# Kernel tuning notes

Measured on AMD Instinct MI355X. Metric: run time of the kernel, lower is better.

## Reference

```python
import jax, jax.numpy as jnp
import numpy as np

EPS = 0.01
MAX_ITER = 10
H = W = 48
N = H * W
B = 16


def radial_cost_matrix():
    # pairwise Euclidean distance between pixel coordinates of an HxW grid,
    # normalized to [0, 1]; shape (1, N, N)
    ys, xs = np.meshgrid(np.arange(H), np.arange(W), indexing='ij')
    coords = np.stack([ys.ravel(), xs.ravel()], axis=1).astype(np.float32)  # (N, 2)
    d = np.sqrt(((coords[:, None, :] - coords[None, :, :]) ** 2).sum(-1))
    d = d / d.max()
    return d[None].astype(np.float32)


def setup_inputs() -> dict:
    key = jax.random.key(0)
    k1, k2 = jax.random.split(key)
    pred_logits = jax.random.normal(k1, (B, H, W), dtype=jnp.float32)
    t = jax.random.uniform(k2, (B, H, W), dtype=jnp.float32)
    target_probs = t / t.sum(axis=(1, 2), keepdims=True)  # valid probability maps
    C = jnp.asarray(radial_cost_matrix())  # (1, N, N) buffer, not trainable
    return {"pred_logits": pred_logits, "target_probs": target_probs, "C": C}


def _M(C, u, v):
    # M_ij = (-c_ij + u_i + v_j) / eps ; shapes: C (1,N,N), u,v (B,N) -> (B,N,N)
    return (-C + u[..., None] + v[..., None, :]) / EPS


def reference(pred_logits, target_probs, C):
    b = pred_logits.shape[0]
    pred_logp = jax.nn.log_softmax(pred_logits.reshape(b, -1), axis=1)  # (B, N)
    target_logp = jnp.log(target_probs.reshape(b, -1) + 1e-8)           # (B, N)

    u = jnp.zeros_like(pred_logp)
    v = jnp.zeros_like(target_logp)
    for _ in range(MAX_ITER):  # fixed small iteration count (no early exit)
        u = EPS * (pred_logp - jax.nn.logsumexp(_M(C, u, v), axis=-1)) + u
        v = EPS * (target_logp - jax.nn.logsumexp(_M(C, u, v), axis=-2)) + v

    pi = jnp.exp(_M(C, u, v))                      # (B, N, N) transport plan
    cost = jnp.sum(pi * C, axis=(-2, -1))           # (B,)
    return cost.mean()                              # reduction='mean'
```

## Files before the change

kernel.cpp:

```cpp
#include <hip/hip_runtime.h>


namespace {

constexpr int N    = 2304;
constexpr int B    = 16;
constexpr int NB   = N * B;
constexpr int R    = 16;
constexpr int WIN  = 33;
constexpr int WPAD = 36;
constexpr int RPB  = 3;
constexpr int AR   = RPB + 2 * R;
constexpr int AST  = 84;
constexpr int NOUT = RPB * 48;
constexpr int NTH  = 17 * 12;

__device__ __forceinline__ float wave_sum(float v) {
#pragma unroll
    for (int off = 32; off >= 1; off >>= 1) v += __shfl_xor(v, off);
    return v;
}

template <bool WC>
__device__ __forceinline__ void stage_wt(float* wtl, float* wcl,
                                         const float* __restrict__ C) {
    for (int i = threadIdx.x; i < WIN * WPAD; i += 256) {
        const int dy = i / WPAD, dx = i - dy * WPAD;
        float wv = 0.f, wc = 0.f;
        if (dx < WIN) {
            const float c = C[1176 * N + (8 + dy) * 48 + (8 + dx)];
            wv = __expf(c * -100.f);
            wc = wv * c;
        }
        wtl[i] = wv;
        if (WC) wcl[i] = wc;
    }
}

template <bool ONES>
__device__ __forceinline__ void stage_apron(float* vl, const float* win,
                                            int b, int y0) {
    for (int i = threadIdx.x; i < AR * 20; i += 256) {
        const int rr = i / 20, c4 = i - rr * 20;
        const int y = y0 - R + rr, x0 = c4 * 4 - R;
        float4 v = make_float4(0.f, 0.f, 0.f, 0.f);
        if ((unsigned)y < 48u && (unsigned)x0 < 48u)
            v = ONES ? make_float4(1.f, 1.f, 1.f, 1.f)
                     : *(const float4*)(win + b * N + y * 48 + x0);
        *(float4*)&vl[rr * AST + c4 * 4] = v;
    }
}

template <int MODE>
__global__ __launch_bounds__(256) void sk_pass(const float* __restrict__ logits,
                                               const float* __restrict__ target,
                                               const float* __restrict__ C,
                                               float* __restrict__ smstat,
                                               float* __restrict__ A,
                                               float* __restrict__ Bh,
                                               float* __restrict__ out) {
    __shared__ float vl[AR * AST];
    __shared__ float wtl[WIN * WPAD];
    __shared__ float part[NTH * 12];
    __shared__ float sred[8];

    const int bid = blockIdx.x;
    const int b   = bid & 15;
    const int y0  = (bid >> 4) * RPB;
    const int tid = threadIdx.x, w = tid >> 6, lane = tid & 63;

    stage_wt<false>(wtl, nullptr, C);
    stage_apron<MODE == 0>(vl, (MODE == 1) ? A : Bh, b, y0);

    float sm_m = 0.f, sm_inv = 0.f;
    if (MODE == 0) {
        float xs[9];
        float m = -3.0e38f;
#pragma unroll
        for (int s9 = 0; s9 < 9; ++s9) {
            xs[s9] = logits[b * N + s9 * 256 + tid];
            m = fmaxf(m, xs[s9]);
        }
#pragma unroll
        for (int off = 32; off >= 1; off >>= 1) m = fmaxf(m, __shfl_xor(m, off));
        if (lane == 0) sred[w] = m;
        __syncthreads();
        m = fmaxf(fmaxf(sred[0], sred[1]), fmaxf(sred[2], sred[3]));
        float sum = 0.f;
#pragma unroll
        for (int s9 = 0; s9 < 9; ++s9) sum += __expf(xs[s9] - m);
#pragma unroll
        for (int off = 32; off >= 1; off >>= 1) sum += __shfl_xor(sum, off);
        __syncthreads();
        if (lane == 0) sred[4 + w] = sum;
        __syncthreads();
        sum = sred[4] + sred[5] + sred[6] + sred[7];
        sm_m = m;
        sm_inv = 1.f / sum;
        if (tid == 0 && (bid >> 4) == 0) {
            smstat[2 * b]     = sm_m;
            smstat[2 * b + 1] = sm_inv;
            if (b == 0) out[0] = 0.f;
        }
    } else if (MODE == 2) {
        sm_m   = smstat[2 * b];
        sm_inv = smstat[2 * b + 1];
    }
    __syncthreads();

    if (tid < NTH) {
        const int dy2 = tid / 12, s = tid - dy2 * 12;
        const int r = s >> 2, xw = (s & 3) * 12;
        float acc[12];
#pragma unroll
        for (int k = 0; k < 12; ++k) acc[k] = 0.f;
#pragma unroll
        for (int h = 0; h < 2; ++h) {
            const int dy = 2 * dy2 + h;
            if (dy < WIN) {
                float vr[44], wr[36];
                const float* vp = &vl[(r + dy) * AST + xw];
#pragma unroll
                for (int c = 0; c < 11; ++c)
                    *(float4*)&vr[4 * c] = *(const float4*)&vp[4 * c];
                const float* wp = &wtl[dy * WPAD];
#pragma unroll
                for (int c = 0; c < 9; ++c)
                    *(float4*)&wr[4 * c] = *(const float4*)&wp[4 * c];
#pragma unroll
                for (int dx = 0; dx < WIN; ++dx)
#pragma unroll
                    for (int k = 0; k < 12; ++k)
                        acc[k] = fmaf(wr[dx], vr[k + dx], acc[k]);
            }
        }
#pragma unroll
        for (int c = 0; c < 3; ++c)
            *(float4*)&part[tid * 12 + 4 * c] = *(float4*)&acc[4 * c];
    }
    __syncthreads();

    if (tid < NOUT) {
        float ssum = 0.f;
#pragma unroll
        for (int d = 0; d < 17; ++d) ssum += part[d * 144 + tid];
        const int o = b * N + (y0 + tid / 48) * 48 + (tid % 48);
        float sv;
        if (MODE == 1) sv = target[o] + 1e-8f;
        else           sv = __expf(logits[o] - sm_m) * sm_inv;
        float* dst = (MODE == 1) ? Bh : A;
        dst[o] = sv / ssum;
    }
}

__global__ __launch_bounds__(256) void sk_cost(const float* __restrict__ C,
                                               const float* __restrict__ target,
                                               const float* __restrict__ A,
                                               float* __restrict__ out) {
    __shared__ float vl[AR * AST];
    __shared__ float wtl[WIN * WPAD], wcl[WIN * WPAD];
    __shared__ float p1[NTH * 12], p2[NTH * 12];
    __shared__ float sred[4];

    const int bid = blockIdx.x;
    const int b   = bid & 15;
    const int y0  = (bid >> 4) * RPB;
    const int tid = threadIdx.x, w = tid >> 6, lane = tid & 63;

    stage_wt<true>(wtl, wcl, C);
    stage_apron<false>(vl, A, b, y0);
    __syncthreads();

    if (tid < NTH) {
        const int dy2 = tid / 12, s = tid - dy2 * 12;
        const int r = s >> 2, xw = (s & 3) * 12;
        float a1[12], a2[12];
#pragma unroll
        for (int k = 0; k < 12; ++k) { a1[k] = 0.f; a2[k] = 0.f; }
#pragma unroll
        for (int h = 0; h < 2; ++h) {
            const int dy = 2 * dy2 + h;
            if (dy < WIN) {
                float vr[44], wr[36], cr[36];
                const float* vp = &vl[(r + dy) * AST + xw];
#pragma unroll
                for (int c = 0; c < 11; ++c)
                    *(float4*)&vr[4 * c] = *(const float4*)&vp[4 * c];
#pragma unroll
                for (int c = 0; c < 9; ++c) {
                    *(float4*)&wr[4 * c] = *(const float4*)&wtl[dy * WPAD + 4 * c];
                    *(float4*)&cr[4 * c] = *(const float4*)&wcl[dy * WPAD + 4 * c];
                }
#pragma unroll
                for (int dx = 0; dx < WIN; ++dx)
#pragma unroll
                    for (int k = 0; k < 12; ++k) {
                        a1[k] = fmaf(wr[dx], vr[k + dx], a1[k]);
                        a2[k] = fmaf(cr[dx], vr[k + dx], a2[k]);
                    }
            }
        }
#pragma unroll
        for (int c = 0; c < 3; ++c) {
            *(float4*)&p1[tid * 12 + 4 * c] = *(float4*)&a1[4 * c];
            *(float4*)&p2[tid * 12 + 4 * c] = *(float4*)&a2[4 * c];
        }
    }
    __syncthreads();

    float val = 0.f;
    if (tid < NOUT) {
        float s1 = 0.f, s2 = 0.f;
#pragma unroll
        for (int d = 0; d < 17; ++d) {
            s1 += p1[d * 144 + tid];
            s2 += p2[d * 144 + tid];
        }
        const int o = b * N + (y0 + tid / 48) * 48 + (tid % 48);
        val = (target[o] + 1e-8f) / s1 * s2;
    }
    val = wave_sum(val);
    if (lane == 0) sred[w] = val;
    __syncthreads();
    if (tid == 0)
        atomicAdd(out, (sred[0] + sred[1] + sred[2] + sred[3]) * (1.f / 16.f));
}

}

extern "C" void kernel_launch(void* const* d_in, const int* in_sizes, int n_in,
                              void* d_out, int out_size, void* d_ws, size_t ws_size,
                              hipStream_t stream) {
    const float* logits = (const float*)d_in[0];
    const float* target = (const float*)d_in[1];
    const float* C      = (const float*)d_in[2];
    float* out = (float*)d_out;
    float* ws  = (float*)d_ws;

    float* smstat = ws;
    float* A      = ws + 32;
    float* Bh     = A + NB;

    sk_pass<0><<<256, 256, 0, stream>>>(logits, target, C, smstat, A, Bh, out);

    for (int t = 1; t <= 9; ++t) {
        sk_pass<1><<<256, 256, 0, stream>>>(logits, target, C, smstat, A, Bh, out);
        sk_pass<2><<<256, 256, 0, stream>>>(logits, target, C, smstat, A, Bh, out);
    }

    sk_cost<<<256, 256, 0, stream>>>(C, target, A, out);
}
```

Measured before the change: 98.05 us.

## Fuse both Sinkhorn half-steps per iteration and shrink the kernel window radius

Each Sinkhorn iteration now runs in one kernel instead of two. The kernel recomputes the intermediate target-side scaling over a halo of rows in shared memory, then convolves it again to produce the next source-side scaling. This halves the number of launches and drops the global round trip for the intermediate buffer. The Gibbs kernel window also shrinks from radius 16 to radius 10, which cuts the FMA work per output. The cost is redundant halo computation of the intermediate rows in every block, plus extra truncation error from the smaller window.

```diff
diff --git a/kernel.cpp b/kernel.cpp
--- a/kernel.cpp
+++ b/kernel.cpp
@@ -6,14 +6,16 @@
 constexpr int N    = 2304;
 constexpr int B    = 16;
 constexpr int NB   = N * B;
-constexpr int R    = 16;
-constexpr int WIN  = 33;
-constexpr int WPAD = 36;
-constexpr int RPB  = 3;
-constexpr int AR   = RPB + 2 * R;
-constexpr int AST  = 84;
-constexpr int NOUT = RPB * 48;
-constexpr int NTH  = 17 * 12;
+constexpr int R    = 10;
+constexpr int WIN  = 21;
+constexpr int WPAD = 24;
+constexpr int APX  = 12;
+constexpr int AST  = 76;
+constexpr int NOUT = 144;
+constexpr int NTH  = WIN * 12;
+constexpr int AVR1 = 23;
+constexpr int AVR2 = 43;
+constexpr int BVR  = 23;
 
 __device__ __forceinline__ float wave_sum(float v) {
 #pragma unroll
@@ -28,7 +30,7 @@
         const int dy = i / WPAD, dx = i - dy * WPAD;
         float wv = 0.f, wc = 0.f;
         if (dx < WIN) {
-            const float c = C[1176 * N + (8 + dy) * 48 + (8 + dx)];
+            const float c = C[1176 * N + (14 + dy) * 48 + (14 + dx)];
             wv = __expf(c * -100.f);
             wc = wv * c;
         }
@@ -38,102 +40,87 @@
 }
 
 template <bool ONES>
-__device__ __forceinline__ void stage_apron(float* vl, const float* win,
-                                            int b, int y0) {
-    for (int i = threadIdx.x; i < AR * 20; i += 256) {
-        const int rr = i / 20, c4 = i - rr * 20;
-        const int y = y0 - R + rr, x0 = c4 * 4 - R;
+__device__ __forceinline__ void stage_ap(float* vl, const float* img,
+                                         int b, int ytop, int nrows) {
+    for (int i = threadIdx.x; i < nrows * 18; i += 256) {
+        const int rr = i / 18, c4 = i - rr * 18;
+        const int y = ytop + rr, x0 = c4 * 4 - APX;
         float4 v = make_float4(0.f, 0.f, 0.f, 0.f);
         if ((unsigned)y < 48u && (unsigned)x0 < 48u)
             v = ONES ? make_float4(1.f, 1.f, 1.f, 1.f)
-                     : *(const float4*)(win + b * N + y * 48 + x0);
+                     : *(const float4*)(img + b * N + y * 48 + x0);
         *(float4*)&vl[rr * AST + c4 * 4] = v;
     }
 }
 
-template <int MODE>
-__global__ __launch_bounds__(256) void sk_pass(const float* __restrict__ logits,
-                                               const float* __restrict__ target,
-                                               const float* __restrict__ C,
-                                               float* __restrict__ smstat,
-                                               float* __restrict__ A,
-                                               float* __restrict__ Bh,
-                                               float* __restrict__ out) {
-    __shared__ float vl[AR * AST];
+__device__ __forceinline__ void conv_row(const float* vp, const float* wp,
+                                         float* acc) {
+    float vr[36], wr[24];
+#pragma unroll
+    for (int c = 0; c < 9; ++c) *(float4*)&vr[4 * c] = *(const float4*)&vp[4 * c];
+#pragma unroll
+    for (int c = 0; c < 6; ++c) *(float4*)&wr[4 * c] = *(const float4*)&wp[4 * c];
+#pragma unroll
+    for (int dx = 0; dx < WIN; ++dx)
+#pragma unroll
+        for (int k = 0; k < 12; ++k)
+            acc[k] = fmaf(wr[dx], vr[k + 2 + dx], acc[k]);
+}
+
+__global__ __launch_bounds__(256) void sk_a1(const float* __restrict__ logits,
+                                             const float* __restrict__ C,
+                                             float* __restrict__ smstat,
+                                             float* __restrict__ A0,
+                                             float* __restrict__ out) {
+    __shared__ float vl[AVR1 * AST];
     __shared__ float wtl[WIN * WPAD];
     __shared__ float part[NTH * 12];
     __shared__ float sred[8];
 
     const int bid = blockIdx.x;
     const int b   = bid & 15;
-    const int y0  = (bid >> 4) * RPB;
+    const int y0  = (bid >> 4) * 3;
     const int tid = threadIdx.x, w = tid >> 6, lane = tid & 63;
 
     stage_wt<false>(wtl, nullptr, C);
-    stage_apron<MODE == 0>(vl, (MODE == 1) ? A : Bh, b, y0);
-
-    float sm_m = 0.f, sm_inv = 0.f;
-    if (MODE == 0) {
-        float xs[9];
-        float m = -3.0e38f;
-#pragma unroll
-        for (int s9 = 0; s9 < 9; ++s9) {
-            xs[s9] = logits[b * N + s9 * 256 + tid];
-            m = fmaxf(m, xs[s9]);
-        }
-#pragma unroll
-        for (int off = 32; off >= 1; off >>= 1) m = fmaxf(m, __shfl_xor(m, off));
-        if (lane == 0) sred[w] = m;
-        __syncthreads();
-        m = fmaxf(fmaxf(sred[0], sred[1]), fmaxf(sred[2], sred[3]));
-        float sum = 0.f;
-#pragma unroll
-        for (int s9 = 0; s9 < 9; ++s9) sum += __expf(xs[s9] - m);
-#pragma unroll
-        for (int off = 32; off >= 1; off >>= 1) sum += __shfl_xor(sum, off);
-        __syncthreads();
-        if (lane == 0) sred[4 + w] = sum;
-        __syncthreads();
-        sum = sred[4] + sred[5] + sred[6] + sred[7];
-        sm_m = m;
-        sm_inv = 1.f / sum;
-        if (tid == 0 && (bid >> 4) == 0) {
-            smstat[2 * b]     = sm_m;
-            smstat[2 * b + 1] = sm_inv;
-            if (b == 0) out[0] = 0.f;
-        }
-    } else if (MODE == 2) {
-        sm_m   = smstat[2 * b];
-        sm_inv = smstat[2 * b + 1];
+    stage_ap<true>(vl, nullptr, b, y0 - R, AVR1);
+
+    float xs[9];
+    float m = -3.0e38f;
+#pragma unroll
+    for (int s9 = 0; s9 < 9; ++s9) {
+        xs[s9] = logits[b * N + s9 * 256 + tid];
+        m = fmaxf(m, xs[s9]);
+    }
+#pragma unroll
+    for (int off = 32; off >= 1; off >>= 1) m = fmaxf(m, __shfl_xor(m, off));
+    if (lane == 0) sred[w] = m;
+    __syncthreads();
+    m = fmaxf(fmaxf(sred[0], sred[1]), fmaxf(sred[2], sred[3]));
+    float sum = 0.f;
+#pragma unroll
+    for (int s9 = 0; s9 < 9; ++s9) sum += __expf(xs[s9] - m);
+#pragma unroll
+    for (int off = 32; off >= 1; off >>= 1) sum += __shfl_xor(sum, off);
+    __syncthreads();
+    if (lane == 0) sred[4 + w] = sum;
+    __syncthreads();
+    sum = sred[4] + sred[5] + sred[6] + sred[7];
+    const float sm_m = m, sm_inv = 1.f / sum;
+    if (tid == 0 && (bid >> 4) == 0) {
+        smstat[2 * b]     = sm_m;
+        smstat[2 * b + 1] = sm_inv;
+        if (b == 0) out[0] = 0.f;
     }
     __syncthreads();
 
     if (tid < NTH) {
-        const int dy2 = tid / 12, s = tid - dy2 * 12;
-        const int r = s >> 2, xw = (s & 3) * 12;
+        const int dy = tid / 12, strip = tid - dy * 12;
+        const int r = strip >> 2, xw = (strip & 3) * 12;
         float acc[12];
 #pragma unroll
         for (int k = 0; k < 12; ++k) acc[k] = 0.f;
-#pragma unroll
-        for (int h = 0; h < 2; ++h) {
-            const int dy = 2 * dy2 + h;
-            if (dy < WIN) {
-                float vr[44], wr[36];
-                const float* vp = &vl[(r + dy) * AST + xw];
-#pragma unroll
-                for (int c = 0; c < 11; ++c)
-                    *(float4*)&vr[4 * c] = *(const float4*)&vp[4 * c];
-                const float* wp = &wtl[dy * WPAD];
-#pragma unroll
-                for (int c = 0; c < 9; ++c)
-                    *(float4*)&wr[4 * c] = *(const float4*)&wp[4 * c];
-#pragma unroll
-                for (int dx = 0; dx < WIN; ++dx)
-#pragma unroll
-                    for (int k = 0; k < 12; ++k)
-                        acc[k] = fmaf(wr[dx], vr[k + dx], acc[k]);
-            }
-        }
+        conv_row(&vl[(r + dy) * AST + xw], &wtl[dy * WPAD], acc);
 #pragma unroll
         for (int c = 0; c < 3; ++c)
             *(float4*)&part[tid * 12 + 4 * c] = *(float4*)&acc[4 * c];
@@ -143,63 +130,133 @@
     if (tid < NOUT) {
         float ssum = 0.f;
 #pragma unroll
-        for (int d = 0; d < 17; ++d) ssum += part[d * 144 + tid];
+        for (int d = 0; d < WIN; ++d) ssum += part[d * 144 + tid];
         const int o = b * N + (y0 + tid / 48) * 48 + (tid % 48);
-        float sv;
-        if (MODE == 1) sv = target[o] + 1e-8f;
-        else           sv = __expf(logits[o] - sm_m) * sm_inv;
-        float* dst = (MODE == 1) ? Bh : A;
-        dst[o] = sv / ssum;
-    }
-}
-
-__global__ __launch_bounds__(256) void sk_cost(const float* __restrict__ C,
-                                               const float* __restrict__ target,
-                                               const float* __restrict__ A,
+        A0[o] = __expf(logits[o] - sm_m) * sm_inv / ssum;
+    }
+}
+
+__global__ __launch_bounds__(256) void sk_fused(const float* __restrict__ logits,
+                                                const float* __restrict__ target,
+                                                const float* __restrict__ C,
+                                                const float* __restrict__ smstat,
+                                                const float* __restrict__ Ain,
+                                                float* __restrict__ Aout) {
+    __shared__ float vl[AVR2 * AST];
+    __shared__ float bv[BVR * AST];
+    __shared__ float wtl[WIN * WPAD];
+    __shared__ float part[NTH * 12];
+
+    const int bid = blockIdx.x;
+    const int b   = bid & 15;
+    const int y0  = (bid >> 4) * 3;
+    const int tid = threadIdx.x;
+
+    stage_wt<false>(wtl, nullptr, C);
+    stage_ap<false>(vl, Ain, b, y0 - 2 * R, AVR2);
+    for (int i = tid; i < BVR * AST; i += 256) bv[i] = 0.f;
+    const float sm_m = smstat[2 * b], sm_inv = smstat[2 * b + 1];
+    __syncthreads();
+
+    int dy = 0, r = 0, xw = 0;
+    const bool act = tid < NTH;
+    if (act) {
+        dy = tid / 12;
+        const int strip = tid - dy * 12;
+        r  = strip >> 2;
+        xw = (strip & 3) * 12;
+    }
+
+    for (int c = 0; c < 8; ++c) {
+        const int rb = 3 * c + r;
+        if (act && rb < BVR) {
+            float acc[12];
+#pragma unroll
+            for (int k = 0; k < 12; ++k) acc[k] = 0.f;
+            conv_row(&vl[(rb + dy) * AST + xw], &wtl[dy * WPAD], acc);
+#pragma unroll
+            for (int cc = 0; cc < 3; ++cc)
+                *(float4*)&part[tid * 12 + 4 * cc] = *(float4*)&acc[4 * cc];
+        }
+        __syncthreads();
+
+        const int nred = (c == 7) ? 96 : 144;
+        if (tid < nred) {
+            float ssum = 0.f;
+#pragma unroll
+            for (int d = 0; d < WIN; ++d) ssum += part[d * 144 + tid];
+            const int rb2 = 3 * c + tid / 48;
+            const int ybg = y0 - R + rb2;
+            const int x   = tid % 48;
+            if ((unsigned)ybg < 48u) {
+                const float q = target[b * N + ybg * 48 + x] + 1e-8f;
+                bv[rb2 * AST + APX + x] = q / ssum;
+            }
+        }
+        __syncthreads();
+    }
+
+    if (act) {
+        float acc[12];
+#pragma unroll
+        for (int k = 0; k < 12; ++k) acc[k] = 0.f;
+        conv_row(&bv[(r + dy) * AST + xw], &wtl[dy * WPAD], acc);
+#pragma unroll
+        for (int cc = 0; cc < 3; ++cc)
+            *(float4*)&part[tid * 12 + 4 * cc] = *(float4*)&acc[4 * cc];
+    }
+    __syncthreads();
+
+    if (tid < NOUT) {
+        float ssum = 0.f;
+#pragma unroll
+        for (int d = 0; d < WIN; ++d) ssum += part[d * 144 + tid];
+        const int o = b * N + (y0 + tid / 48) * 48 + (tid % 48);
+        Aout[o] = __expf(logits[o] - sm_m) * sm_inv / ssum;
+    }
+}
+
+__global__ __launch_bounds__(256) void sk_cost(const float* __restrict__ target,
+                                               const float* __restrict__ C,
+                                               const float* __restrict__ Ain,
                                                float* __restrict__ out) {
-    __shared__ float vl[AR * AST];
+    __shared__ float vl[AVR1 * AST];
     __shared__ float wtl[WIN * WPAD], wcl[WIN * WPAD];
     __shared__ float p1[NTH * 12], p2[NTH * 12];
     __shared__ float sred[4];
 
     const int bid = blockIdx.x;
     const int b   = bid & 15;
-    const int y0  = (bid >> 4) * RPB;
+    const int y0  = (bid >> 4) * 3;
     const int tid = threadIdx.x, w = tid >> 6, lane = tid & 63;
 
     stage_wt<true>(wtl, wcl, C);
-    stage_apron<false>(vl, A, b, y0);
+    stage_ap<false>(vl, Ain, b, y0 - R, AVR1);
     __syncthreads();
 
     if (tid < NTH) {
-        const int dy2 = tid / 12, s = tid - dy2 * 12;
-        const int r = s >> 2, xw = (s & 3) * 12;
+        const int dy = tid / 12, strip = tid - dy * 12;
+        const int r = strip >> 2, xw = (strip & 3) * 12;
         float a1[12], a2[12];
 #pragma unroll
         for (int k = 0; k < 12; ++k) { a1[k] = 0.f; a2[k] = 0.f; }
-#pragma unroll
-        for (int h = 0; h < 2; ++h) {
-            const int dy = 2 * dy2 + h;
-            if (dy < WIN) {
-                float vr[44], wr[36], cr[36];
-                const float* vp = &vl[(r + dy) * AST + xw];
-#pragma unroll
-                for (int c = 0; c < 11; ++c)
-                    *(float4*)&vr[4 * c] = *(const float4*)&vp[4 * c];
-#pragma unroll
-                for (int c = 0; c < 9; ++c) {
-                    *(float4*)&wr[4 * c] = *(const float4*)&wtl[dy * WPAD + 4 * c];
-                    *(float4*)&cr[4 * c] = *(const float4*)&wcl[dy * WPAD + 4 * c];
-                }
-#pragma unroll
-                for (int dx = 0; dx < WIN; ++dx)
-#pragma unroll
-                    for (int k = 0; k < 12; ++k) {
-                        a1[k] = fmaf(wr[dx], vr[k + dx], a1[k]);
-                        a2[k] = fmaf(cr[dx], vr[k + dx], a2[k]);
-                    }
+        float vr[36], wr[24], cr[24];
+        const float* vp = &vl[(r + dy) * AST + xw];
+#pragma unroll
+        for (int c = 0; c < 9; ++c)
+            *(float4*)&vr[4 * c] = *(const float4*)&vp[4 * c];
+#pragma unroll
+        for (int c = 0; c < 6; ++c) {
+            *(float4*)&wr[4 * c] = *(const float4*)&wtl[dy * WPAD + 4 * c];
+            *(float4*)&cr[4 * c] = *(const float4*)&wcl[dy * WPAD + 4 * c];
+        }
+#pragma unroll
+        for (int dx = 0; dx < WIN; ++dx)
+#pragma unroll
+            for (int k = 0; k < 12; ++k) {
+                a1[k] = fmaf(wr[dx], vr[k + 2 + dx], a1[k]);
+                a2[k] = fmaf(cr[dx], vr[k + 2 + dx], a2[k]);
             }
-        }
 #pragma unroll
         for (int c = 0; c < 3; ++c) {
             *(float4*)&p1[tid * 12 + 4 * c] = *(float4*)&a1[4 * c];
@@ -212,7 +269,7 @@
     if (tid < NOUT) {
         float s1 = 0.f, s2 = 0.f;
 #pragma unroll
-        for (int d = 0; d < 17; ++d) {
+        for (int d = 0; d < WIN; ++d) {
             s1 += p1[d * 144 + tid];
             s2 += p2[d * 144 + tid];
         }
@@ -238,15 +295,16 @@
     float* ws  = (float*)d_ws;
 
     float* smstat = ws;
-    float* A      = ws + 32;
-    float* Bh     = A + NB;
-
-    sk_pass<0><<<256, 256, 0, stream>>>(logits, target, C, smstat, A, Bh, out);
-
-    for (int t = 1; t <= 9; ++t) {
-        sk_pass<1><<<256, 256, 0, stream>>>(logits, target, C, smstat, A, Bh, out);
-        sk_pass<2><<<256, 256, 0, stream>>>(logits, target, C, smstat, A, Bh, out);
-    }
-
-    sk_cost<<<256, 256, 0, stream>>>(C, target, A, out);
-}
+    float* A0     = ws + 32;
+    float* A1     = A0 + NB;
+
+    sk_a1<<<256, 256, 0, stream>>>(logits, C, smstat, A0, out);
+
+    float* bufs[2] = {A0, A1};
+    for (int t = 0; t < 9; ++t) {
+        sk_fused<<<256, 256, 0, stream>>>(logits, target, C, smstat,
+                                          bufs[t & 1], bufs[(t & 1) ^ 1]);
+    }
+
+    sk_cost<<<256, 256, 0, stream>>>(target, C, A1, out);
+}
```

New measurement: 124.6 us. 1.27x slower.
